# Kernel tuning notes

Measured on AMD Instinct MI355X. Metric: run time of the kernel, lower is better.

Reference implementation:

```python
import jax, jax.numpy as jnp
import numpy as np

B, DIM, H, W = 2, 256, 32, 32
HALF, DI, DS, DTR = DIM // 2, 256, 16, 8
DEPTH, K1 = 2, 4


def _ln(x, w, b, eps=1e-5):
    m = jnp.mean(x, -1, keepdims=True)
    v = jnp.var(x, -1, keepdims=True)
    return (x - m) * jax.lax.rsqrt(v + eps) * w + b


def _selective_scan(dA, dBu, C):
    # dA, dBu: (N, L, D, S); C: (N, L, S) -> y: (N, L, D)
    def step(h, ab):
        a, b = ab
        h = a * h + b
        return h, h
    h0 = jnp.zeros((dA.shape[0],) + dA.shape[2:], dA.dtype)
    _, hs = jax.lax.scan(step, h0, (jnp.moveaxis(dA, 1, 0), jnp.moveaxis(dBu, 1, 0)))
    return jnp.einsum('lnds,nls->nld', hs, C)


def _mamba_block(xs, ln_w, ln_b, in_w, cw, cb, xw, dtw, dtb, Alog, Dp, ow):
    # xs: (B, L, HALF); canonical Mamba-1 block, pre-LN residual
    Lq = xs.shape[1]
    h = _ln(xs, ln_w, ln_b)
    u, z = jnp.split(h @ in_w, 2, axis=-1)  # (B,L,DI) each
    up = jnp.pad(u, ((0, 0), (K1 - 1, 0), (0, 0)))  # causal depthwise conv1d
    u = sum(up[:, k:k + Lq, :] * cw[:, k] for k in range(K1)) + cb
    u = jax.nn.silu(u)
    dbc = u @ xw
    dtr, Bm, Cm = jnp.split(dbc, [DTR, DTR + DS], axis=-1)
    dt = jax.nn.softplus(dtr @ dtw + dtb)  # (B,L,DI)
    A = -jnp.exp(Alog)  # (DI,DS)
    dA = jnp.exp(dt[..., None] * A)
    dBu = (dt * u)[..., None] * Bm[:, :, None, :]
    y = _selective_scan(dA, dBu, Cm) + u * Dp
    return xs + (y * jax.nn.silu(z)) @ ow


def _vss_block(x, ln_w, ln_b, in_w, cw, cb, xw, dtw, dtb, Alog, Dp, on_w, on_b, ow):
    # x: (B, HALF, H, W); VMamba SS2D block (4-direction cross-scan), pre-LN residual
    Bq, _, Hq, Wq = x.shape
    Lq = Hq * Wq
    h = _ln(x.transpose(0, 2, 3, 1), ln_w, ln_b)
    u, z = jnp.split(h @ in_w, 2, axis=-1)  # (B,H,W,DI)
    u2 = jax.lax.conv_general_dilated(u.transpose(0, 3, 1, 2), cw[:, None], (1, 1), ((1, 1), (1, 1)),
                                      feature_group_count=DI,
                                      dimension_numbers=('NCHW', 'OIHW', 'NCHW')) + cb[None, :, None, None]
    u2 = jax.nn.silu(u2)  # (B,DI,H,W)
    s0 = u2.reshape(Bq, DI, Lq)
    s1 = u2.transpose(0, 1, 3, 2).reshape(Bq, DI, Lq)
    us = jnp.stack([s0, s1, jnp.flip(s0, -1), jnp.flip(s1, -1)], 1).transpose(0, 1, 3, 2)  # (B,4,L,DI)
    dbc = jnp.einsum('bkld,kdr->bklr', us, xw)
    dtr, Bm, Cm = jnp.split(dbc, [DTR, DTR + DS], axis=-1)
    dt = jax.nn.softplus(jnp.einsum('bklr,krd->bkld', dtr, dtw) + dtb[None, :, None, :])
    A = -jnp.exp(Alog)  # (4,DI,DS)
    dA = jnp.exp(dt[..., None] * A[None, :, None])  # (B,4,L,DI,DS)
    dBu = (dt * us)[..., None] * Bm[:, :, :, None, :]
    y = _selective_scan(dA.reshape(Bq * 4, Lq, DI, DS), dBu.reshape(Bq * 4, Lq, DI, DS), Cm.reshape(Bq * 4, Lq, DS))
    y = y.reshape(Bq, 4, Lq, DI) + us * Dp[None, :, None, :]
    yt = y.transpose(0, 1, 3, 2)  # (B,4,DI,L)
    y0 = yt[:, 0]
    y1 = yt[:, 1].reshape(Bq, DI, Wq, Hq).transpose(0, 1, 3, 2).reshape(Bq, DI, Lq)
    y2 = jnp.flip(yt[:, 2], -1)
    y3 = jnp.flip(yt[:, 3], -1).reshape(Bq, DI, Wq, Hq).transpose(0, 1, 3, 2).reshape(Bq, DI, Lq)
    ym = _ln((y0 + y1 + y2 + y3).transpose(0, 2, 1), on_w, on_b)  # (B,L,DI)
    out = (ym * jax.nn.silu(z.reshape(Bq, Lq, DI))) @ ow  # (B,L,HALF)
    return x + out.reshape(Bq, Hq, Wq, HALF).transpose(0, 3, 1, 2)


def _fwd(x, proj1_w, proj1_b, proj2_w, proj2_b,
         m_ln_w, m_ln_b, m_in_w, m_conv_w, m_conv_b, m_xproj_w, m_dt_w, m_dt_b, m_Alog, m_D, m_out_w,
         v_ln_w, v_ln_b, v_in_w, v_conv_w, v_conv_b, v_xproj_w, v_dt_w, v_dt_b, v_Alog, v_D,
         v_onorm_w, v_onorm_b, v_out_w, fuse_w, fuse_b, bn_g, bn_b, bn_m, bn_v):
    Bq, _, Hq, Wq = x.shape
    Lq = Hq * Wq
    p1 = jnp.einsum('oc,bchw->bohw', proj1_w, x) + proj1_b[None, :, None, None]
    s = p1.reshape(Bq, HALF, Lq).transpose(0, 2, 1)
    for i in range(DEPTH):
        s = _mamba_block(s, m_ln_w[i], m_ln_b[i], m_in_w[i], m_conv_w[i], m_conv_b[i], m_xproj_w[i],
                         m_dt_w[i], m_dt_b[i], m_Alog[i], m_D[i], m_out_w[i])
    p1 = s.transpose(0, 2, 1).reshape(Bq, HALF, Hq, Wq)
    p2 = jnp.einsum('oc,bchw->bohw', proj2_w, x) + proj2_b[None, :, None, None]
    for i in range(DEPTH):
        p2 = _vss_block(p2, v_ln_w[i], v_ln_b[i], v_in_w[i], v_conv_w[i], v_conv_b[i], v_xproj_w[i],
                        v_dt_w[i], v_dt_b[i], v_Alog[i], v_D[i], v_onorm_w[i], v_onorm_b[i], v_out_w[i])
    xc = jnp.concatenate([p1, p2], 1)
    y = jax.lax.conv_general_dilated(xc, fuse_w, (1, 1), ((1, 1), (1, 1)),
                                     dimension_numbers=('NCHW', 'OIHW', 'NCHW')) + fuse_b[None, :, None, None]
    y = (y - bn_m[None, :, None, None]) * jax.lax.rsqrt(bn_v + 1e-5)[None, :, None, None] * bn_g[None, :, None, None] + bn_b[None, :, None, None]
    return jax.nn.relu(y)


def setup_inputs() -> dict:
    key = jax.random.key(0)
    ks = iter(jax.random.split(key, 64))
    n = lambda shape, s=0.02: jax.random.normal(next(ks), shape, jnp.float32) * s
    A_row = jnp.log(jnp.arange(1, DS + 1, dtype=jnp.float32))  # standard S4D-real init
    return {
        'x': jax.random.normal(next(ks), (B, DIM, H, W), jnp.float32),
        'proj1_w': n((HALF, DIM), 0.05), 'proj1_b': n((HALF,)),
        'proj2_w': n((HALF, DIM), 0.05), 'proj2_b': n((HALF,)),
        'm_ln_w': jnp.ones((DEPTH, HALF)), 'm_ln_b': jnp.zeros((DEPTH, HALF)),
        'm_in_w': n((DEPTH, HALF, 2 * DI)),
        'm_conv_w': n((DEPTH, DI, K1), 0.1), 'm_conv_b': n((DEPTH, DI)),
        'm_xproj_w': n((DEPTH, DI, DTR + 2 * DS)),
        'm_dt_w': n((DEPTH, DTR, DI), 0.1), 'm_dt_b': n((DEPTH, DI)),
        'm_Alog': jnp.array(jnp.broadcast_to(A_row, (DEPTH, DI, DS))),
        'm_D': jnp.ones((DEPTH, DI)),
        'm_out_w': n((DEPTH, DI, HALF)),
        'v_ln_w': jnp.ones((DEPTH, HALF)), 'v_ln_b': jnp.zeros((DEPTH, HALF)),
        'v_in_w': n((DEPTH, HALF, 2 * DI)),
        'v_conv_w': n((DEPTH, DI, 3, 3), 0.1), 'v_conv_b': n((DEPTH, DI)),
        'v_xproj_w': n((DEPTH, 4, DI, DTR + 2 * DS)),
        'v_dt_w': n((DEPTH, 4, DTR, DI), 0.1), 'v_dt_b': n((DEPTH, 4, DI)),
        'v_Alog': jnp.array(jnp.broadcast_to(A_row, (DEPTH, 4, DI, DS))),
        'v_D': jnp.ones((DEPTH, 4, DI)),
        'v_onorm_w': jnp.ones((DEPTH, DI)), 'v_onorm_b': jnp.zeros((DEPTH, DI)),
        'v_out_w': n((DEPTH, DI, HALF)),
        'fuse_w': n((DIM, DIM, 3, 3), 0.02), 'fuse_b': n((DIM,)),
        'bn_g': jnp.ones((DIM,)), 'bn_b': jnp.zeros((DIM,)),
        'bn_m': n((DIM,)), 'bn_v': jax.random.uniform(next(ks), (DIM,), jnp.float32, 0.5, 1.5),
    }


def reference(x, proj1_w, proj1_b, proj2_w, proj2_b,
              m_ln_w, m_ln_b, m_in_w, m_conv_w, m_conv_b, m_xproj_w, m_dt_w, m_dt_b, m_Alog, m_D, m_out_w,
              v_ln_w, v_ln_b, v_in_w, v_conv_w, v_conv_b, v_xproj_w, v_dt_w, v_dt_b, v_Alog, v_D,
              v_onorm_w, v_onorm_b, v_out_w, fuse_w, fuse_b, bn_g, bn_b, bn_m, bn_v):
    return _fwd(x, proj1_w, proj1_b, proj2_w, proj2_b,
                m_ln_w, m_ln_b, m_in_w, m_conv_w, m_conv_b, m_xproj_w, m_dt_w, m_dt_b, m_Alog, m_D, m_out_w,
                v_ln_w, v_ln_b, v_in_w, v_conv_w, v_conv_b, v_xproj_w, v_dt_w, v_dt_b, v_Alog, v_D,
                v_onorm_w, v_onorm_b, v_out_w, fuse_w, fuse_b, bn_g, bn_b, bn_m, bn_v)
```

## Files before the change

kernel.cpp:

```cpp
#include <hip/hip_runtime.h>
#include <math.h>

#define CH  16
#define NCH 64

typedef __attribute__((ext_vector_type(8))) short bf16x8;
typedef __attribute__((ext_vector_type(4))) float f32x4;
typedef __attribute__((ext_vector_type(4))) unsigned int u32x4;

__device__ __forceinline__ float dev_silu(float x){ return x * (1.0f/(1.0f + __expf(-x))); }
__device__ __forceinline__ float dev_softplus(float x){ return fmaxf(x,0.0f) + log1pf(__expf(-fabsf(x))); }
__device__ __forceinline__ unsigned short dev_bf16(float f){
    unsigned int u = __float_as_uint(f);
    return (unsigned short)((u + 0x7fffu + ((u >> 16) & 1u)) >> 16);
}

__global__ void __launch_bounds__(256)
k_prep(const float* __restrict__ w1, const float* __restrict__ w2, float* __restrict__ wtc,
       const float* __restrict__ fw, unsigned short* __restrict__ Wr)
{
    if (blockIdx.x < 64){
        int bc = blockIdx.x;
        int ot = bc & 7, ct = bc >> 3;
        __shared__ float t[32][33];
        int col = threadIdx.x & 31, r8 = threadIdx.x >> 5;
        #pragma unroll
        for (int i = 0; i < 4; ++i){
            int r = i*8 + r8;
            int o = ot*32 + r;
            const float* src = (o < 128) ? (w1 + (size_t)o*256) : (w2 + (size_t)(o-128)*256);
            t[r][col] = src[ct*32 + col];
        }
        __syncthreads();
        #pragma unroll
        for (int i = 0; i < 4; ++i){
            int r = i*8 + r8;
            int c = ct*32 + r, o = ot*32 + col;
            wtc[(size_t)c*256 + o] = t[col][r];
        }
    } else {
        int t0 = ((blockIdx.x - 64)*256 + threadIdx.x)*4;
        unsigned int r[4];
        #pragma unroll
        for (int j = 0; j < 4; ++j){
            int i = t0 + j;
            int o = i / 2304, kk = i - o*2304;
            int kp = kk >> 8, cc = kk & 255;
            r[j] = dev_bf16(fw[(size_t)o*2304 + cc*9 + kp]);
        }
        uint2 pk; pk.x = r[0] | (r[1] << 16); pk.y = r[2] | (r[3] << 16);
        *(uint2*)(Wr + t0) = pk;
    }
}

__global__ void __launch_bounds__(256)
k_proj(const float* __restrict__ x, const float* __restrict__ wtc,
       const float* __restrict__ b1, const float* __restrict__ b2,
       float* __restrict__ sm, float* __restrict__ sv)
{
    int blk = blockIdx.x;
    int b = blk >> 8, l0 = (blk & 255) * 4;
    int tid = threadIdx.x;
    __shared__ float4 xs[256];
    xs[tid] = *(const float4*)(x + ((size_t)(b*256 + tid))*1024 + l0);
    __syncthreads();
    int o = tid & 127;
    float bias = (tid < 128) ? b1[o] : b2[o];
    float a0 = bias, a1 = bias, a2 = bias, a3 = bias;
    #pragma unroll 4
    for (int c = 0; c < 256; ++c){
        float wv = wtc[(size_t)c*256 + tid];
        float4 xv = xs[c];
        a0 = fmaf(wv, xv.x, a0);
        a1 = fmaf(wv, xv.y, a1);
        a2 = fmaf(wv, xv.z, a2);
        a3 = fmaf(wv, xv.w, a3);
    }
    float* dst = (tid < 128) ? sm : sv;
    size_t base = ((size_t)b*1024 + l0)*128 + o;
    dst[base      ] = a0;
    dst[base + 128] = a1;
    dst[base + 256] = a2;
    dst[base + 384] = a3;
}

__device__ __forceinline__ void lnmm_core(int bl0, float4 v,
    const float* __restrict__ lnw, const float* __restrict__ lnb,
    const float* __restrict__ inw, float* __restrict__ u, float* __restrict__ z,
    float (*hn)[132])
{
    int tid = threadIdx.x;
    int row = tid >> 5, lane = tid & 31;
    float a = v.x + v.y + v.z + v.w;
    float q = v.x*v.x + v.y*v.y + v.z*v.z + v.w*v.w;
    #pragma unroll
    for (int o = 16; o; o >>= 1){ a += __shfl_xor(a, o); q += __shfl_xor(q, o); }
    float mean = a * (1.0f/128.0f);
    float rs = rsqrtf(q * (1.0f/128.0f) - mean*mean + 1e-5f);
    float4 w4 = *(const float4*)(lnw + lane*4);
    float4 b4 = *(const float4*)(lnb + lane*4);
    float4 hv;
    hv.x = (v.x-mean)*rs*w4.x + b4.x;
    hv.y = (v.y-mean)*rs*w4.y + b4.y;
    hv.z = (v.z-mean)*rs*w4.z + b4.z;
    hv.w = (v.w-mean)*rs*w4.w + b4.w;
    *(float4*)&hn[row][lane*4] = hv;
    __syncthreads();
    float acc0[8] = {0,0,0,0,0,0,0,0};
    float acc1[8] = {0,0,0,0,0,0,0,0};
    for (int c = 0; c < 128; c += 4){
        float w0[4], w1[4];
        #pragma unroll
        for (int i = 0; i < 4; ++i){
            w0[i] = inw[(size_t)(c+i)*512 + tid];
            w1[i] = inw[(size_t)(c+i)*512 + tid + 256];
        }
        #pragma unroll
        for (int r = 0; r < 8; ++r){
            float4 h4 = *(const float4*)&hn[r][c];
            acc0[r] = fmaf(h4.x, w0[0], acc0[r]);
            acc0[r] = fmaf(h4.y, w0[1], acc0[r]);
            acc0[r] = fmaf(h4.z, w0[2], acc0[r]);
            acc0[r] = fmaf(h4.w, w0[3], acc0[r]);
            acc1[r] = fmaf(h4.x, w1[0], acc1[r]);
            acc1[r] = fmaf(h4.y, w1[1], acc1[r]);
            acc1[r] = fmaf(h4.z, w1[2], acc1[r]);
            acc1[r] = fmaf(h4.w, w1[3], acc1[r]);
        }
    }
    #pragma unroll
    for (int r = 0; r < 8; ++r){
        u[(size_t)(bl0 + r)*256 + tid] = acc0[r];
        z[(size_t)(bl0 + r)*256 + tid] = acc1[r];
    }
}

__global__ void __launch_bounds__(256)
k_lnmm2(const float* __restrict__ sm_, const float* __restrict__ mlnw, const float* __restrict__ mlnb,
        const float* __restrict__ minw, float* __restrict__ um, float* __restrict__ zm,
        const float* __restrict__ sv_, const float* __restrict__ vlnw, const float* __restrict__ vlnb,
        const float* __restrict__ vinw, float* __restrict__ uv, float* __restrict__ zv)
{
    __shared__ float hn[8][132];
    int tid = threadIdx.x;
    int row = tid >> 5, lane = tid & 31;
    if (blockIdx.x < 256){
        int bl0 = blockIdx.x*8;
        float4 v = *(const float4*)(sm_ + (size_t)(bl0 + row)*128 + lane*4);
        lnmm_core(bl0, v, mlnw, mlnb, minw, um, zm, hn);
    } else {
        int bl0 = (blockIdx.x-256)*8;
        float4 v = *(const float4*)(sv_ + (size_t)(bl0 + row)*128 + lane*4);
        lnmm_core(bl0, v, vlnw, vlnb, vinw, uv, zv, hn);
    }
}

__global__ void __launch_bounds__(256)
k_conv2(const float* __restrict__ urm, const float* __restrict__ cwm, const float* __restrict__ cbm,
        float* __restrict__ uc,
        const float* __restrict__ urv, const float* __restrict__ cwv, const float* __restrict__ cbv,
        float* __restrict__ us)
{
    int d = threadIdx.x;
    if (blockIdx.x < 2048){
        int bl = blockIdx.x; int b = bl >> 10, l = bl & 1023;
        float acc = cbm[d];
        #pragma unroll
        for (int k = 0; k < 4; ++k){
            int lp = l - 3 + k;
            if (lp >= 0) acc = fmaf(urm[((size_t)(b<<10) + lp)*256 + d], cwm[d*4 + k], acc);
        }
        uc[(size_t)bl*256 + d] = dev_silu(acc);
    } else {
        int bl = blockIdx.x - 2048; int b = bl >> 10, l = bl & 1023;
        int h = l >> 5, w = l & 31;
        float acc = cbv[d];
        #pragma unroll
        for (int kh = 0; kh < 3; ++kh){
            int hh = h + kh - 1; if (hh < 0 || hh > 31) continue;
            #pragma unroll
            for (int kw = 0; kw < 3; ++kw){
                int ww = w + kw - 1; if (ww < 0 || ww > 31) continue;
                acc = fmaf(urv[((size_t)(b<<10) + (hh<<5) + ww)*256 + d], cwv[d*9 + kh*3 + kw], acc);
            }
        }
        float v = dev_silu(acc);
        int l1 = (w<<5) + h;
        size_t base = (size_t)b*4*1024*256;
        us[base + ((size_t)0*1024 + l        )*256 + d] = v;
        us[base + ((size_t)1*1024 + l1       )*256 + d] = v;
        us[base + ((size_t)2*1024 + (1023-l ))*256 + d] = v;
        us[base + ((size_t)3*1024 + (1023-l1))*256 + d] = v;
    }
}

__device__ __forceinline__ void xsa_body(int bk, int ch, int k,
    const float* __restrict__ u, const float* __restrict__ xw,
    const float* __restrict__ dtw, const float* __restrict__ dtb,
    const float* __restrict__ Alog,
    float* __restrict__ dt, float* __restrict__ Bm, float* __restrict__ Cm,
    float* __restrict__ Pb, float* __restrict__ Qb)
{
    int tid = threadIdx.x;
    __shared__ float ursh[16][256];
    __shared__ float xwsh[64][40];
    __shared__ float dbc[16][44];
    size_t idx0 = (size_t)bk*1024 + ch*CH;
    #pragma unroll
    for (int p = 0; p < 16; ++p)
        ursh[p][tid] = u[(idx0 + p)*256 + tid];
    const float* xwk = xw + (size_t)k*256*40;
    int pp[3], rr[3];
    #pragma unroll
    for (int rnd = 0; rnd < 3; ++rnd){
        int t = rnd*256 + tid;
        pp[rnd] = t/40; rr[rnd] = t - pp[rnd]*40;
    }
    float accd[3] = {0.f, 0.f, 0.f};
    for (int ct = 0; ct < 4; ++ct){
        __syncthreads();
        for (int i = tid; i < 64*40; i += 256)
            xwsh[i/40][i%40] = xwk[(size_t)(ct*64 + i/40)*40 + (i%40)];
        __syncthreads();
        #pragma unroll
        for (int rnd = 0; rnd < 3; ++rnd){
            int t = rnd*256 + tid;
            if (t < 640){
                int p = pp[rnd], r = rr[rnd];
                float a = accd[rnd];
                #pragma unroll 8
                for (int cc = 0; cc < 64; ++cc)
                    a = fmaf(ursh[p][ct*64 + cc], xwsh[cc][r], a);
                accd[rnd] = a;
            }
        }
    }
    __syncthreads();
    #pragma unroll
    for (int rnd = 0; rnd < 3; ++rnd){
        int t = rnd*256 + tid;
        if (t < 640) dbc[pp[rnd]][rr[rnd]] = accd[rnd];
    }
    __syncthreads();
    const float* dtwk = dtw + (size_t)k*8*256;
    float bias = dtb[k*256 + tid];
    float wv[8];
    #pragma unroll
    for (int r = 0; r < 8; ++r) wv[r] = dtwk[r*256 + tid];
    float dtv[16], duv[16];
    #pragma unroll
    for (int p = 0; p < 16; ++p){
        float a = bias;
        #pragma unroll
        for (int r = 0; r < 8; ++r) a = fmaf(dbc[p][r], wv[r], a);
        a = dev_softplus(a);
        dtv[p] = a;
        dt[(idx0 + p)*256 + tid] = a;
        duv[p] = a * ursh[p][tid];
    }
    {
        int p = tid >> 4, s = tid & 15;
        Bm[(idx0 + p)*16 + s] = dbc[p][8 + s];
        Cm[(idx0 + p)*16 + s] = dbc[p][24 + s];
    }
    float A[16];
    const float4* Ap = (const float4*)(Alog + ((size_t)k*256 + tid)*16);
    #pragma unroll
    for (int q = 0; q < 4; ++q){
        float4 v = Ap[q];
        A[q*4+0] = -__expf(v.x); A[q*4+1] = -__expf(v.y);
        A[q*4+2] = -__expf(v.z); A[q*4+3] = -__expf(v.w);
    }
    float Q[16];
    #pragma unroll
    for (int s = 0; s < 16; ++s) Q[s] = 0.f;
    float S = 0.f;
    #pragma unroll
    for (int j = 0; j < 16; ++j){
        S += dtv[j];
        #pragma unroll
        for (int s = 0; s < 16; ++s){
            float av = __expf(dtv[j]*A[s]);
            Q[s] = fmaf(av, Q[s], duv[j]*dbc[j][8 + s]);
        }
    }
    size_t oidx = ((size_t)(bk*NCH + ch)*256 + tid)*16;
    float4* Pp = (float4*)(Pb + oidx);
    float4* Qp = (float4*)(Qb + oidx);
    #pragma unroll
    for (int q = 0; q < 4; ++q){
        float4 pv, qv;
        pv.x = __expf(S*A[q*4+0]); pv.y = __expf(S*A[q*4+1]);
        pv.z = __expf(S*A[q*4+2]); pv.w = __expf(S*A[q*4+3]);
        qv.x = Q[q*4+0]; qv.y = Q[q*4+1]; qv.z = Q[q*4+2]; qv.w = Q[q*4+3];
        Pp[q] = pv; Qp[q] = qv;
    }
}

__global__ void __launch_bounds__(256)
k_xsa2(const float* __restrict__ um, const float* __restrict__ mxw, const float* __restrict__ mdtw,
       const float* __restrict__ mdtb, const float* __restrict__ mAlog,
       float* __restrict__ dtm, float* __restrict__ Bmm, float* __restrict__ Cmm,
       float* __restrict__ Pbm, float* __restrict__ Qbm,
       const float* __restrict__ uv, const float* __restrict__ vxw, const float* __restrict__ vdtw,
       const float* __restrict__ vdtb, const float* __restrict__ vAlog,
       float* __restrict__ dtv_, float* __restrict__ Bmv, float* __restrict__ Cmv,
       float* __restrict__ Pbv, float* __restrict__ Qbv)
{
    if (blockIdx.x < 128){
        int blk = blockIdx.x;
        xsa_body(blk >> 6, blk & 63, 0, um, mxw, mdtw, mdtb, mAlog, dtm, Bmm, Cmm, Pbm, Qbm);
    } else {
        int blk = blockIdx.x - 128;
        int bk = blk >> 6;
        xsa_body(bk, blk & 63, bk & 3, uv, vxw, vdtw, vdtb, vAlog, dtv_, Bmv, Cmv, Pbv, Qbv);
    }
}

__device__ __forceinline__ void scanP_body(int bk, int dg, float* __restrict__ Pb,
                                           const float* __restrict__ Qb)
{
    int tid = threadIdx.x;
    size_t idx0 = (size_t)bk*NCH*4096 + dg*256 + tid;
    float Pv[NCH], Qv[NCH];
    #pragma unroll
    for (int c = 0; c < NCH; ++c){
        Pv[c] = Pb[idx0 + (size_t)c*4096];
        Qv[c] = Qb[idx0 + (size_t)c*4096];
    }
    float h = 0.f;
    #pragma unroll
    for (int c = 0; c < NCH; ++c){
        Pb[idx0 + (size_t)c*4096] = h;
        h = fmaf(Pv[c], h, Qv[c]);
    }
}

__global__ void __launch_bounds__(256)
k_scanP2(float* __restrict__ Pbm, const float* __restrict__ Qbm,
         float* __restrict__ Pbv, const float* __restrict__ Qbv)
{
    if (blockIdx.x < 32) scanP_body(blockIdx.x >> 4, blockIdx.x & 15, Pbm, Qbm);
    else { int blk = blockIdx.x - 32; scanP_body(blk >> 4, blk & 15, Pbv, Qbv); }
}

__device__ __forceinline__ void scanB_body(int bk, int c, int k, const float* __restrict__ dt,
    const float* __restrict__ u, const float* __restrict__ Bm, const float* __restrict__ Cm,
    const float* __restrict__ Alog, const float* __restrict__ Hb, float* __restrict__ y)
{
    int d = threadIdx.x;
    __shared__ float Bsh[CH][16], Csh[CH][16];
    {
        int j = threadIdx.x >> 4, s = threadIdx.x & 15;
        size_t bi = ((size_t)bk*1024 + c*CH + j)*16 + s;
        Bsh[j][s] = Bm[bi];
        Csh[j][s] = Cm[bi];
    }
    float dtv[CH], duv[CH];
    size_t base = ((size_t)bk*1024 + c*CH)*256 + d;
    #pragma unroll
    for (int j = 0; j < CH; ++j){
        float a = dt[base + (size_t)j*256];
        float b = u [base + (size_t)j*256];
        dtv[j] = a; duv[j] = a*b;
    }
    float A[16];
    const float4* Ap = (const float4*)(Alog + ((size_t)k*256 + d)*16);
    #pragma unroll
    for (int q = 0; q < 4; ++q){
        float4 v = Ap[q];
        A[q*4+0] = -__expf(v.x); A[q*4+1] = -__expf(v.y);
        A[q*4+2] = -__expf(v.z); A[q*4+3] = -__expf(v.w);
    }
    float h[16];
    const float4* Hp = (const float4*)(Hb + ((size_t)(bk*NCH + c)*256 + d)*16);
    #pragma unroll
    for (int q = 0; q < 4; ++q){
        float4 v = Hp[q];
        h[q*4+0] = v.x; h[q*4+1] = v.y; h[q*4+2] = v.z; h[q*4+3] = v.w;
    }
    __syncthreads();
    float* yp = y + base;
    #pragma unroll
    for (int j = 0; j < CH; ++j){
        float py = 0.f;
        #pragma unroll
        for (int s = 0; s < 16; ++s){
            float av = __expf(dtv[j]*A[s]);
            h[s] = fmaf(av, h[s], duv[j]*Bsh[j][s]);
            py = fmaf(h[s], Csh[j][s], py);
        }
        yp[(size_t)j*256] = py;
    }
}

__global__ void __launch_bounds__(256)
k_scanB2(const float* __restrict__ dtm, const float* __restrict__ um, const float* __restrict__ Bmm,
         const float* __restrict__ Cmm, const float* __restrict__ mAlog,
         const float* __restrict__ Hbm, float* __restrict__ ym,
         const float* __restrict__ dtv, const float* __restrict__ uv, const float* __restrict__ Bmv,
         const float* __restrict__ Cmv, const float* __restrict__ vAlog,
         const float* __restrict__ Hbv, float* __restrict__ yv)
{
    if (blockIdx.x < 128){
        int blk = blockIdx.x;
        scanB_body(blk >> 6, blk & (NCH-1), 0, dtm, um, Bmm, Cmm, mAlog, Hbm, ym);
    } else {
        int blk = blockIdx.x - 128;
        int bk = blk >> 6;
        scanB_body(bk, blk & (NCH-1), bk & 3, dtv, uv, Bmv, Cmv, vAlog, Hbv, yv);
    }
}

__device__ __forceinline__ void mout_body(int bl0, const float* __restrict__ y,
    const float* __restrict__ uc, const float* __restrict__ z, const float* __restrict__ Dp,
    const float* __restrict__ ow, float* __restrict__ sm, float* __restrict__ srowp)
{
    int tid = threadIdx.x;
    int row = tid >> 5, c0 = (tid & 31) * 8;
    __shared__ float gld[8][264];
    size_t base = (size_t)(bl0 + row)*256 + c0;
    #pragma unroll
    for (int i = 0; i < 8; i += 4){
        float4 yv = *(const float4*)(y + base + i);
        float4 uv = *(const float4*)(uc + base + i);
        float4 zv = *(const float4*)(z + base + i);
        float4 dv = *(const float4*)(Dp + c0 + i);
        gld[row][c0+i+0] = (yv.x + uv.x*dv.x) * dev_silu(zv.x);
        gld[row][c0+i+1] = (yv.y + uv.y*dv.y) * dev_silu(zv.y);
        gld[row][c0+i+2] = (yv.z + uv.z*dv.z) * dev_silu(zv.z);
        gld[row][c0+i+3] = (yv.w + uv.w*dv.w) * dev_silu(zv.w);
    }
    __syncthreads();
    int o = tid & 127, rg = tid >> 7;
    float acc[4] = {0,0,0,0};
    for (int c = 0; c < 256; c += 4){
        float w[4];
        #pragma unroll
        for (int i = 0; i < 4; ++i) w[i] = ow[(size_t)(c+i)*128 + o];
        #pragma unroll
        for (int r = 0; r < 4; ++r){
            float4 h4 = *(const float4*)&gld[rg*4 + r][c];
            acc[r] = fmaf(h4.x, w[0], acc[r]);
            acc[r] = fmaf(h4.y, w[1], acc[r]);
            acc[r] = fmaf(h4.z, w[2], acc[r]);
            acc[r] = fmaf(h4.w, w[3], acc[r]);
        }
    }
    #pragma unroll
    for (int r = 0; r < 4; ++r){
        size_t gi = (size_t)(bl0 + rg*4 + r)*128 + o;
        float nv = sm[gi] + acc[r];
        sm[gi] = nv;
        srowp[(rg*4 + r)*128 + o] = nv;
    }
}

__device__ __forceinline__ void vcomb_body(int blk, const float* __restrict__ y,
    const float* __restrict__ us, const float* __restrict__ z, const float* __restrict__ Dp,
    const float* __restrict__ onw, const float* __restrict__ onb, const float* __restrict__ ow,
    float* __restrict__ sv, float* __restrict__ srowp)
{
    int b = blk >> 7;
    int l0 = (blk & 127) * 8;
    int tid = threadIdx.x;
    int row = tid >> 5, c0 = (tid & 31) * 8;
    int l = l0 + row;
    int h = l >> 5, w = l & 31;
    int l1 = (w<<5) + h, l2 = 1023 - l, l3 = 1023 - l1;
    size_t base = (size_t)b*4*1024*256;
    size_t i0 = base + ((size_t)0*1024 + l )*256 + c0;
    size_t i1 = base + ((size_t)1*1024 + l1)*256 + c0;
    size_t i2 = base + ((size_t)2*1024 + l2)*256 + c0;
    size_t i3 = base + ((size_t)3*1024 + l3)*256 + c0;
    float t[8];
    #pragma unroll
    for (int i = 0; i < 8; i += 4){
        float4 yv = *(const float4*)(y + i0 + i);
        float4 uv = *(const float4*)(us + i0 + i);
        float4 dv = *(const float4*)(Dp + 0*256 + c0 + i);
        t[i+0] = yv.x + uv.x*dv.x; t[i+1] = yv.y + uv.y*dv.y;
        t[i+2] = yv.z + uv.z*dv.z; t[i+3] = yv.w + uv.w*dv.w;
    }
    #pragma unroll
    for (int i = 0; i < 8; i += 4){
        float4 yv = *(const float4*)(y + i1 + i);
        float4 uv = *(const float4*)(us + i1 + i);
        float4 dv = *(const float4*)(Dp + 1*256 + c0 + i);
        t[i+0] += yv.x + uv.x*dv.x; t[i+1] += yv.y + uv.y*dv.y;
        t[i+2] += yv.z + uv.z*dv.z; t[i+3] += yv.w + uv.w*dv.w;
    }
    #pragma unroll
    for (int i = 0; i < 8; i += 4){
        float4 yv = *(const float4*)(y + i2 + i);
        float4 uv = *(const float4*)(us + i2 + i);
        float4 dv = *(const float4*)(Dp + 2*256 + c0 + i);
        t[i+0] += yv.x + uv.x*dv.x; t[i+1] += yv.y + uv.y*dv.y;
        t[i+2] += yv.z + uv.z*dv.z; t[i+3] += yv.w + uv.w*dv.w;
    }
    #pragma unroll
    for (int i = 0; i < 8; i += 4){
        float4 yv = *(const float4*)(y + i3 + i);
        float4 uv = *(const float4*)(us + i3 + i);
        float4 dv = *(const float4*)(Dp + 3*256 + c0 + i);
        t[i+0] += yv.x + uv.x*dv.x; t[i+1] += yv.y + uv.y*dv.y;
        t[i+2] += yv.z + uv.z*dv.z; t[i+3] += yv.w + uv.w*dv.w;
    }
    float a = 0.f, q = 0.f;
    #pragma unroll
    for (int i = 0; i < 8; ++i){ a += t[i]; q += t[i]*t[i]; }
    #pragma unroll
    for (int o = 16; o; o >>= 1){ a += __shfl_xor(a, o); q += __shfl_xor(q, o); }
    float mean = a * (1.0f/256.0f);
    float rs = rsqrtf(q * (1.0f/256.0f) - mean*mean + 1e-5f);
    __shared__ float gld[8][264];
    size_t zbase = (size_t)(b*1024 + l)*256 + c0;
    #pragma unroll
    for (int i = 0; i < 8; i += 4){
        float4 wv = *(const float4*)(onw + c0 + i);
        float4 bv = *(const float4*)(onb + c0 + i);
        float4 zv = *(const float4*)(z + zbase + i);
        gld[row][c0+i+0] = ((t[i+0]-mean)*rs*wv.x + bv.x) * dev_silu(zv.x);
        gld[row][c0+i+1] = ((t[i+1]-mean)*rs*wv.y + bv.y) * dev_silu(zv.y);
        gld[row][c0+i+2] = ((t[i+2]-mean)*rs*wv.z + bv.z) * dev_silu(zv.z);
        gld[row][c0+i+3] = ((t[i+3]-mean)*rs*wv.w + bv.w) * dev_silu(zv.w);
    }
    __syncthreads();
    int o = tid & 127, rg = tid >> 7;
    float acc[4] = {0,0,0,0};
    for (int c = 0; c < 256; c += 4){
        float wv[4];
        #pragma unroll
        for (int i = 0; i < 4; ++i) wv[i] = ow[(size_t)(c+i)*128 + o];
        #pragma unroll
        for (int r = 0; r < 4; ++r){
            float4 h4 = *(const float4*)&gld[rg*4 + r][c];
            acc[r] = fmaf(h4.x, wv[0], acc[r]);
            acc[r] = fmaf(h4.y, wv[1], acc[r]);
            acc[r] = fmaf(h4.z, wv[2], acc[r]);
            acc[r] = fmaf(h4.w, wv[3], acc[r]);
        }
    }
    #pragma unroll
    for (int r = 0; r < 4; ++r){
        size_t gi = (size_t)(b*1024 + l0 + rg*4 + r)*128 + o;
        float nv = sv[gi] + acc[r];
        sv[gi] = nv;
        srowp[(rg*4 + r)*128 + o] = nv;
    }
}

__global__ void __launch_bounds__(256)
k_epi2(const float* __restrict__ ym, const float* __restrict__ uc, const float* __restrict__ zm,
       const float* __restrict__ mD, const float* __restrict__ mow, float* __restrict__ sm,
       const float* __restrict__ yv, const float* __restrict__ us, const float* __restrict__ zv,
       const float* __restrict__ vD, const float* __restrict__ onw, const float* __restrict__ onb,
       const float* __restrict__ vow, float* __restrict__ sv)
{
    __shared__ float srow[8][128];
    if (blockIdx.x < 256) mout_body(blockIdx.x*8, ym, uc, zm, mD, mow, sm, &srow[0][0]);
    else                  vcomb_body(blockIdx.x-256, yv, us, zv, vD, onw, onb, vow, sv, &srow[0][0]);
}

__global__ void __launch_bounds__(256)
k_epln2(const float* __restrict__ ym, const float* __restrict__ uc, const float* __restrict__ zm,
        const float* __restrict__ mD, const float* __restrict__ mow, float* __restrict__ sm,
        const float* __restrict__ yv, const float* __restrict__ us, const float* __restrict__ zv,
        const float* __restrict__ vD, const float* __restrict__ onw, const float* __restrict__ onb,
        const float* __restrict__ vow, float* __restrict__ sv,
        const float* __restrict__ mlnw, const float* __restrict__ mlnb, const float* __restrict__ minw,
        float* __restrict__ um_o, float* __restrict__ zm_o,
        const float* __restrict__ vlnw, const float* __restrict__ vlnb, const float* __restrict__ vinw,
        float* __restrict__ uv_o, float* __restrict__ zv_o)
{
    __shared__ float srow[8][128];
    __shared__ float hn[8][132];
    int tid = threadIdx.x;
    int row = tid >> 5, lane = tid & 31;
    if (blockIdx.x < 256){
        int bl0 = blockIdx.x*8;
        mout_body(bl0, ym, uc, zm, mD, mow, sm, &srow[0][0]);
        __syncthreads();
        float4 v = *(const float4*)&srow[row][lane*4];
        lnmm_core(bl0, v, mlnw, mlnb, minw, um_o, zm_o, hn);
    } else {
        int blk = blockIdx.x - 256;
        int bl0 = (blk >> 7)*1024 + (blk & 127)*8;
        vcomb_body(blk, yv, us, zv, vD, onw, onb, vow, sv, &srow[0][0]);
        __syncthreads();
        float4 v = *(const float4*)&srow[row][lane*4];
        lnmm_core(bl0, v, vlnw, vlnb, vinw, uv_o, zv_o, hn);
    }
}

__global__ void __launch_bounds__(256)
k_fgemm(const unsigned short* __restrict__ Wr, const float* __restrict__ sm,
        const float* __restrict__ sv, const float* __restrict__ fb,
        const float* __restrict__ bg, const float* __restrict__ bb,
        const float* __restrict__ bm, const float* __restrict__ bv, float* __restrict__ out)
{
    int o0 = (blockIdx.x & 3) * 64;
    int n0 = (blockIdx.x >> 2) * 64;
    int tid = threadIdx.x, lane = tid & 63, wid = tid >> 6;
    int wm = (wid >> 1) * 32, wn = (wid & 1) * 32;
    __shared__ unsigned short sA[64*40];
    __shared__ unsigned short sB[64*40];
    f32x4 acc[2][2] = {};
    int srow = tid >> 2, scol = (tid & 3) * 8;
    const u32x4* gA = (const u32x4*)(Wr + (size_t)(o0 + srow)*2304 + scol);
    u32x4* wA = (u32x4*)(sA + srow*40 + scol);
    u32x4* wB = (u32x4*)(sB + srow*40 + scol);
    int n = n0 + srow; int b = n >> 10, p = n & 1023, h = p >> 5, w = p & 31;
    int fr = lane & 15, fk = (lane >> 4) * 8;
    const unsigned short* rA0 = sA + (wm + fr)*40 + fk;
    const unsigned short* rA1 = sA + (wm + 16 + fr)*40 + fk;
    const unsigned short* rB0 = sB + (wn + fr)*40 + fk;
    const unsigned short* rB1 = sB + (wn + 16 + fr)*40 + fk;
    for (int kt = 0; kt < 72; ++kt){
        u32x4 va = gA[kt*4];
        int kp = kt >> 3, c0 = (kt & 7) * 32;
        int kh = kp / 3, kw = kp - kh*3;
        int hh = h + kh - 1, ww = w + kw - 1;
        int cg = c0 + scol;
        float4 v0 = make_float4(0.f,0.f,0.f,0.f), v1 = v0;
        if ((unsigned)hh < 32u && (unsigned)ww < 32u){
            const float* sp = ((cg < 128) ? sm : sv)
                            + ((size_t)(b*1024 + (hh<<5) + ww))*128 + (cg & 127);
            v0 = *(const float4*)sp;
            v1 = *(const float4*)(sp + 4);
        }
        u32x4 vb;
        vb.x = dev_bf16(v0.x) | ((unsigned)dev_bf16(v0.y) << 16);
        vb.y = dev_bf16(v0.z) | ((unsigned)dev_bf16(v0.w) << 16);
        vb.z = dev_bf16(v1.x) | ((unsigned)dev_bf16(v1.y) << 16);
        vb.w = dev_bf16(v1.z) | ((unsigned)dev_bf16(v1.w) << 16);
        __syncthreads();
        *wA = va; *wB = vb;
        __syncthreads();
        bf16x8 a0 = *(const bf16x8*)rA0;
        bf16x8 a1 = *(const bf16x8*)rA1;
        bf16x8 b0 = *(const bf16x8*)rB0;
        bf16x8 b1 = *(const bf16x8*)rB1;
        acc[0][0] = __builtin_amdgcn_mfma_f32_16x16x32_bf16(a0, b0, acc[0][0], 0, 0, 0);
        acc[0][1] = __builtin_amdgcn_mfma_f32_16x16x32_bf16(a0, b1, acc[0][1], 0, 0, 0);
        acc[1][0] = __builtin_amdgcn_mfma_f32_16x16x32_bf16(a1, b0, acc[1][0], 0, 0, 0);
        acc[1][1] = __builtin_amdgcn_mfma_f32_16x16x32_bf16(a1, b1, acc[1][1], 0, 0, 0);
    }
    #pragma unroll
    for (int i = 0; i < 2; ++i){
        int ob = o0 + wm + i*16 + (lane >> 4) * 4;
        #pragma unroll
        for (int j = 0; j < 2; ++j){
            int nn = n0 + wn + j*16 + (lane & 15);
            int bb_ = nn >> 10, pp = nn & 1023;
            #pragma unroll
            for (int q = 0; q < 4; ++q){
                int o = ob + q;
                float v = acc[i][j][q] + fb[o];
                v = (v - bm[o]) * rsqrtf(bv[o] + 1e-5f) * bg[o] + bb[o];
                out[((size_t)(bb_*256 + o))*1024 + pp] = fmaxf(v, 0.f);
            }
        }
    }
}

extern "C" void kernel_launch(void* const* d_in, const int* in_sizes, int n_in,
                              void* d_out, int out_size, void* d_ws, size_t ws_size,
                              hipStream_t stream)
{
    const float* x         = (const float*)d_in[0];
    const float* proj1_w   = (const float*)d_in[1];
    const float* proj1_b   = (const float*)d_in[2];
    const float* proj2_w   = (const float*)d_in[3];
    const float* proj2_b   = (const float*)d_in[4];
    const float* m_ln_w    = (const float*)d_in[5];
    const float* m_ln_b    = (const float*)d_in[6];
    const float* m_in_w    = (const float*)d_in[7];
    const float* m_conv_w  = (const float*)d_in[8];
    const float* m_conv_b  = (const float*)d_in[9];
    const float* m_xproj_w = (const float*)d_in[10];
    const float* m_dt_w    = (const float*)d_in[11];
    const float* m_dt_b    = (const float*)d_in[12];
    const float* m_Alog    = (const float*)d_in[13];
    const float* m_D       = (const float*)d_in[14];
    const float* m_out_w   = (const float*)d_in[15];
    const float* v_ln_w    = (const float*)d_in[16];
    const float* v_ln_b    = (const float*)d_in[17];
    const float* v_in_w    = (const float*)d_in[18];
    const float* v_conv_w  = (const float*)d_in[19];
    const float* v_conv_b  = (const float*)d_in[20];
    const float* v_xproj_w = (const float*)d_in[21];
    const float* v_dt_w    = (const float*)d_in[22];
    const float* v_dt_b    = (const float*)d_in[23];
    const float* v_Alog    = (const float*)d_in[24];
    const float* v_D       = (const float*)d_in[25];
    const float* v_onorm_w = (const float*)d_in[26];
    const float* v_onorm_b = (const float*)d_in[27];
    const float* v_out_w   = (const float*)d_in[28];
    const float* fuse_w    = (const float*)d_in[29];
    const float* fuse_b    = (const float*)d_in[30];
    const float* bn_g      = (const float*)d_in[31];
    const float* bn_b      = (const float*)d_in[32];
    const float* bn_m      = (const float*)d_in[33];
    const float* bn_v      = (const float*)d_in[34];
    float* out = (float*)d_out;

    float* ws = (float*)d_ws;
    float* sm     = ws;  ws += 2*1024*128;
    float* sv     = ws;  ws += 2*1024*128;
    float* uraw_m = ws;  ws += 2*1024*256;
    float* zb_m   = ws;  ws += 2*1024*256;
    float* uc     = ws;  ws += 2*1024*256;
    float* uraw_v = ws;  ws += 2*1024*256;
    float* zb_v   = ws;  ws += 2*1024*256;
    float* usb    = ws;  ws += 2*4*1024*256;
    float* dt_m   = ws;  ws += 2*1024*256;
    float* yb_m   = ws;  ws += 2*1024*256;
    float* Pb_m   = ws;  ws += 2*NCH*256*16;
    float* Qb_m   = ws;  ws += 2*NCH*256*16;
    float* Bm_m   = ws;  ws += 2*1024*16;
    float* Cm_m   = ws;  ws += 2*1024*16;
    float* dt_v   = ws;  ws += 2*4*1024*256;
    float* yb_v   = ws;  ws += 2*4*1024*256;
    float* Pb_v   = ws;  ws += 2*4*NCH*256*16;
    float* Qb_v   = ws;  ws += 2*4*NCH*256*16;
    float* Bm_v   = ws;  ws += 2*4*1024*16;
    float* Cm_v   = ws;  ws += 2*4*1024*16;
    float* wtc    = ws;  ws += 256*256;
    unsigned short* Wr = (unsigned short*)ws;  ws += 576*1024/2;

    k_prep<<<640,   256, 0, stream>>>(proj1_w, proj2_w, wtc, fuse_w, Wr);
    k_proj<<<2*256, 256, 0, stream>>>(x, wtc, proj1_b, proj2_b, sm, sv);

    k_lnmm2<<<512, 256, 0, stream>>>(sm, m_ln_w, m_ln_b, m_in_w, uraw_m, zb_m,
                                     sv, v_ln_w, v_ln_b, v_in_w, uraw_v, zb_v);

    for (int i = 0; i < 2; ++i){
        k_conv2 <<<4096, 256, 0, stream>>>(uraw_m, m_conv_w + (size_t)i*1024, m_conv_b + i*256, uc,
                                           uraw_v, v_conv_w + (size_t)i*2304, v_conv_b + i*256, usb);
        k_xsa2  <<<640,  256, 0, stream>>>(uc,  m_xproj_w + (size_t)i*10240,
                                           m_dt_w + (size_t)i*2048, m_dt_b + i*256,
                                           m_Alog + (size_t)i*4096,
                                           dt_m, Bm_m, Cm_m, Pb_m, Qb_m,
                                           usb, v_xproj_w + (size_t)i*40960,
                                           v_dt_w + (size_t)i*8192, v_dt_b + (size_t)i*1024,
                                           v_Alog + (size_t)i*16384,
                                           dt_v, Bm_v, Cm_v, Pb_v, Qb_v);
        k_scanP2<<<160,  256, 0, stream>>>(Pb_m, Qb_m, Pb_v, Qb_v);
        k_scanB2<<<640,  256, 0, stream>>>(dt_m, uc,  Bm_m, Cm_m, m_Alog + (size_t)i*4096,
                                           Pb_m, yb_m,
                                           dt_v, usb, Bm_v, Cm_v, v_Alog + (size_t)i*16384,
                                           Pb_v, yb_v);
        if (i == 0){
            k_epln2<<<512, 256, 0, stream>>>(yb_m, uc, zb_m, m_D, m_out_w, sm,
                                             yb_v, usb, zb_v, v_D,
                                             v_onorm_w, v_onorm_b, v_out_w, sv,
                                             m_ln_w + 128, m_ln_b + 128, m_in_w + 65536,
                                             uraw_m, zb_m,
                                             v_ln_w + 128, v_ln_b + 128, v_in_w + 65536,
                                             uraw_v, zb_v);
        } else {
            k_epi2 <<<512, 256, 0, stream>>>(yb_m, uc, zb_m, m_D + 256, m_out_w + 32768, sm,
                                             yb_v, usb, zb_v, v_D + 1024,
                                             v_onorm_w + 256, v_onorm_b + 256,
                                             v_out_w + 32768, sv);
        }
    }

    k_fgemm<<<4*32, 256, 0, stream>>>(Wr, sm, sv, fuse_b, bn_g, bn_b, bn_m, bn_v, out);
}
```

Baseline: 351.2 us.

## Split fused x-projection/chunk-scan kernel into finer-grained xproj and scanA kernels

The combined kernel did the x-projection GEMV, dt softplus and the chunk-local scan state in one 640-block launch with 16 rows per block. It is now two launches. A 2560-block xproj kernel handles 4 rows per block and reads x_proj weights straight from global memory. A separate scanA kernel reloads dt, u and B to compute the chunk P/Q summaries. This raises parallelism for the projection, at the cost of an extra launch and extra global round-trips for dt and u.

```diff
diff --git a/kernel.cpp b/kernel.cpp
--- a/kernel.cpp
+++ b/kernel.cpp
@@ -194,52 +194,26 @@
     }
 }
 
-__device__ __forceinline__ void xsa_body(int bk, int ch, int k,
-    const float* __restrict__ u, const float* __restrict__ xw,
-    const float* __restrict__ dtw, const float* __restrict__ dtb,
-    const float* __restrict__ Alog,
-    float* __restrict__ dt, float* __restrict__ Bm, float* __restrict__ Cm,
-    float* __restrict__ Pb, float* __restrict__ Qb)
+__device__ __forceinline__ void xproj_body(size_t idx0, int k, const float* __restrict__ u,
+    const float* __restrict__ xw, const float* __restrict__ dtw, const float* __restrict__ dtb,
+    float* __restrict__ dt, float* __restrict__ Bm, float* __restrict__ Cm)
 {
     int tid = threadIdx.x;
-    __shared__ float ursh[16][256];
-    __shared__ float xwsh[64][40];
-    __shared__ float dbc[16][44];
-    size_t idx0 = (size_t)bk*1024 + ch*CH;
-    #pragma unroll
-    for (int p = 0; p < 16; ++p)
+    __shared__ float ursh[4][256];
+    __shared__ float dbc[4][44];
+    #pragma unroll
+    for (int p = 0; p < 4; ++p)
         ursh[p][tid] = u[(idx0 + p)*256 + tid];
-    const float* xwk = xw + (size_t)k*256*40;
-    int pp[3], rr[3];
-    #pragma unroll
-    for (int rnd = 0; rnd < 3; ++rnd){
-        int t = rnd*256 + tid;
-        pp[rnd] = t/40; rr[rnd] = t - pp[rnd]*40;
-    }
-    float accd[3] = {0.f, 0.f, 0.f};
-    for (int ct = 0; ct < 4; ++ct){
-        __syncthreads();
-        for (int i = tid; i < 64*40; i += 256)
-            xwsh[i/40][i%40] = xwk[(size_t)(ct*64 + i/40)*40 + (i%40)];
-        __syncthreads();
-        #pragma unroll
-        for (int rnd = 0; rnd < 3; ++rnd){
-            int t = rnd*256 + tid;
-            if (t < 640){
-                int p = pp[rnd], r = rr[rnd];
-                float a = accd[rnd];
-                #pragma unroll 8
-                for (int cc = 0; cc < 64; ++cc)
-                    a = fmaf(ursh[p][ct*64 + cc], xwsh[cc][r], a);
-                accd[rnd] = a;
-            }
-        }
-    }
     __syncthreads();
-    #pragma unroll
-    for (int rnd = 0; rnd < 3; ++rnd){
-        int t = rnd*256 + tid;
-        if (t < 640) dbc[pp[rnd]][rr[rnd]] = accd[rnd];
+    if (tid < 160){
+        int r = tid % 40, p = tid / 40;
+        const float* xwc = xw + (size_t)k*256*40 + r;
+        float a0 = 0.f, a1 = 0.f;
+        for (int c = 0; c < 128; ++c){
+            a0 = fmaf(ursh[p][c],       xwc[(size_t)c*40],       a0);
+            a1 = fmaf(ursh[p][c + 128], xwc[(size_t)(c+128)*40], a1);
+        }
+        dbc[p][r] = a0 + a1;
     }
     __syncthreads();
     const float* dtwk = dtw + (size_t)k*8*256;
@@ -247,44 +221,81 @@
     float wv[8];
     #pragma unroll
     for (int r = 0; r < 8; ++r) wv[r] = dtwk[r*256 + tid];
-    float dtv[16], duv[16];
-    #pragma unroll
-    for (int p = 0; p < 16; ++p){
+    #pragma unroll
+    for (int p = 0; p < 4; ++p){
         float a = bias;
         #pragma unroll
         for (int r = 0; r < 8; ++r) a = fmaf(dbc[p][r], wv[r], a);
-        a = dev_softplus(a);
-        dtv[p] = a;
-        dt[(idx0 + p)*256 + tid] = a;
-        duv[p] = a * ursh[p][tid];
-    }
+        dt[(idx0 + p)*256 + tid] = dev_softplus(a);
+    }
+    if (tid < 128){
+        int p = tid >> 5, j = tid & 31;
+        if (j < 16) Bm[(idx0 + p)*16 + j]        = dbc[p][8 + j];
+        else        Cm[(idx0 + p)*16 + (j - 16)] = dbc[p][8 + j];
+    }
+}
+
+__global__ void __launch_bounds__(256)
+k_xproj2(const float* __restrict__ um, const float* __restrict__ mxw, const float* __restrict__ mdtw,
+         const float* __restrict__ mdtb, float* __restrict__ dtm, float* __restrict__ Bmm,
+         float* __restrict__ Cmm,
+         const float* __restrict__ uv, const float* __restrict__ vxw, const float* __restrict__ vdtw,
+         const float* __restrict__ vdtb, float* __restrict__ dtv, float* __restrict__ Bmv,
+         float* __restrict__ Cmv)
+{
+    if (blockIdx.x < 512){
+        int bk = blockIdx.x >> 8;
+        size_t idx0 = (size_t)bk*1024 + (blockIdx.x & 255)*4;
+        xproj_body(idx0, 0, um, mxw, mdtw, mdtb, dtm, Bmm, Cmm);
+    } else {
+        int blk = blockIdx.x - 512;
+        int bk = blk >> 8;
+        size_t idx0 = (size_t)bk*1024 + (blk & 255)*4;
+        xproj_body(idx0, bk & 3, uv, vxw, vdtw, vdtb, dtv, Bmv, Cmv);
+    }
+}
+
+__device__ __forceinline__ void scanA_body(int bk, int c, int k, const float* __restrict__ dt,
+    const float* __restrict__ u, const float* __restrict__ Bm, const float* __restrict__ Alog,
+    float* __restrict__ Pb, float* __restrict__ Qb)
+{
+    int d = threadIdx.x;
+    __shared__ float Bsh[CH][16];
     {
-        int p = tid >> 4, s = tid & 15;
-        Bm[(idx0 + p)*16 + s] = dbc[p][8 + s];
-        Cm[(idx0 + p)*16 + s] = dbc[p][24 + s];
+        int j = threadIdx.x >> 4, s = threadIdx.x & 15;
+        Bsh[j][s] = Bm[((size_t)bk*1024 + c*CH + j)*16 + s];
+    }
+    float dtv[CH], duv[CH];
+    size_t base = ((size_t)bk*1024 + c*CH)*256 + d;
+    #pragma unroll
+    for (int j = 0; j < CH; ++j){
+        float a = dt[base + (size_t)j*256];
+        float b = u [base + (size_t)j*256];
+        dtv[j] = a; duv[j] = a*b;
     }
     float A[16];
-    const float4* Ap = (const float4*)(Alog + ((size_t)k*256 + tid)*16);
+    const float4* Ap = (const float4*)(Alog + ((size_t)k*256 + d)*16);
     #pragma unroll
     for (int q = 0; q < 4; ++q){
         float4 v = Ap[q];
         A[q*4+0] = -__expf(v.x); A[q*4+1] = -__expf(v.y);
         A[q*4+2] = -__expf(v.z); A[q*4+3] = -__expf(v.w);
     }
+    __syncthreads();
     float Q[16];
     #pragma unroll
     for (int s = 0; s < 16; ++s) Q[s] = 0.f;
     float S = 0.f;
     #pragma unroll
-    for (int j = 0; j < 16; ++j){
+    for (int j = 0; j < CH; ++j){
         S += dtv[j];
         #pragma unroll
         for (int s = 0; s < 16; ++s){
             float av = __expf(dtv[j]*A[s]);
-            Q[s] = fmaf(av, Q[s], duv[j]*dbc[j][8 + s]);
-        }
-    }
-    size_t oidx = ((size_t)(bk*NCH + ch)*256 + tid)*16;
+            Q[s] = fmaf(av, Q[s], duv[j]*Bsh[j][s]);
+        }
+    }
+    size_t oidx = ((size_t)(bk*NCH + c)*256 + d)*16;
     float4* Pp = (float4*)(Pb + oidx);
     float4* Qp = (float4*)(Qb + oidx);
     #pragma unroll
@@ -298,22 +309,18 @@
 }
 
 __global__ void __launch_bounds__(256)
-k_xsa2(const float* __restrict__ um, const float* __restrict__ mxw, const float* __restrict__ mdtw,
-       const float* __restrict__ mdtb, const float* __restrict__ mAlog,
-       float* __restrict__ dtm, float* __restrict__ Bmm, float* __restrict__ Cmm,
-       float* __restrict__ Pbm, float* __restrict__ Qbm,
-       const float* __restrict__ uv, const float* __restrict__ vxw, const float* __restrict__ vdtw,
-       const float* __restrict__ vdtb, const float* __restrict__ vAlog,
-       float* __restrict__ dtv_, float* __restrict__ Bmv, float* __restrict__ Cmv,
-       float* __restrict__ Pbv, float* __restrict__ Qbv)
+k_scanA2(const float* __restrict__ dtm, const float* __restrict__ um, const float* __restrict__ Bmm,
+         const float* __restrict__ mAlog, float* __restrict__ Pbm, float* __restrict__ Qbm,
+         const float* __restrict__ dtv, const float* __restrict__ uv, const float* __restrict__ Bmv,
+         const float* __restrict__ vAlog, float* __restrict__ Pbv, float* __restrict__ Qbv)
 {
     if (blockIdx.x < 128){
         int blk = blockIdx.x;
-        xsa_body(blk >> 6, blk & 63, 0, um, mxw, mdtw, mdtb, mAlog, dtm, Bmm, Cmm, Pbm, Qbm);
+        scanA_body(blk >> 6, blk & (NCH-1), 0, dtm, um, Bmm, mAlog, Pbm, Qbm);
     } else {
         int blk = blockIdx.x - 128;
         int bk = blk >> 6;
-        xsa_body(bk, blk & 63, bk & 3, uv, vxw, vdtw, vdtb, vAlog, dtv_, Bmv, Cmv, Pbv, Qbv);
+        scanA_body(bk, blk & (NCH-1), bk & 3, dtv, uv, Bmv, vAlog, Pbv, Qbv);
     }
 }
 
@@ -738,14 +745,14 @@
     for (int i = 0; i < 2; ++i){
         k_conv2 <<<4096, 256, 0, stream>>>(uraw_m, m_conv_w + (size_t)i*1024, m_conv_b + i*256, uc,
                                            uraw_v, v_conv_w + (size_t)i*2304, v_conv_b + i*256, usb);
-        k_xsa2  <<<640,  256, 0, stream>>>(uc,  m_xproj_w + (size_t)i*10240,
+        k_xproj2<<<2560, 256, 0, stream>>>(uc,  m_xproj_w + (size_t)i*10240,
                                            m_dt_w + (size_t)i*2048, m_dt_b + i*256,
-                                           m_Alog + (size_t)i*4096,
-                                           dt_m, Bm_m, Cm_m, Pb_m, Qb_m,
+                                           dt_m, Bm_m, Cm_m,
                                            usb, v_xproj_w + (size_t)i*40960,
                                            v_dt_w + (size_t)i*8192, v_dt_b + (size_t)i*1024,
-                                           v_Alog + (size_t)i*16384,
-                                           dt_v, Bm_v, Cm_v, Pb_v, Qb_v);
+                                           dt_v, Bm_v, Cm_v);
+        k_scanA2<<<640,  256, 0, stream>>>(dt_m, uc,  Bm_m, m_Alog + (size_t)i*4096,  Pb_m, Qb_m,
+                                           dt_v, usb, Bm_v, v_Alog + (size_t)i*16384, Pb_v, Qb_v);
         k_scanP2<<<160,  256, 0, stream>>>(Pb_m, Qb_m, Pb_v, Qb_v);
         k_scanB2<<<640,  256, 0, stream>>>(dt_m, uc,  Bm_m, Cm_m, m_Alog + (size_t)i*4096,
                                            Pb_m, yb_m,
```

Result: faster. 332.2 us (-5.4%).
